# Kernel tuning notes

Measured on AMD Instinct MI355X. Metric: run time of the kernel, lower is better.

The kernel has to match this reference:

```python
import jax, jax.numpy as jnp
import numpy as np

NUM_BRANCHES = 4
REP_DIM = 1024
FEAT_DIM = 128
N_DATA = 100000
NCE_K = 4096
NCE_T = 0.07
BATCH = 128
EPS = 1e-07


def setup_inputs() -> dict:
    key = jax.random.key(0)
    ks = jax.random.split(key, 8)
    d = {}
    for i in range(NUM_BRANCHES):
        d[f"emb{i}"] = jax.random.normal(ks[i], (BATCH, REP_DIM), dtype=jnp.float32)
    d["W"] = jax.random.normal(ks[4], (NUM_BRANCHES, FEAT_DIM, REP_DIM), dtype=jnp.float32) * 0.03
    d["b"] = jnp.zeros((NUM_BRANCHES, FEAT_DIM), dtype=jnp.float32)
    stdv = 1.0 / np.sqrt(FEAT_DIM / 3.0)
    d["memory"] = jax.random.uniform(ks[5], (NUM_BRANCHES, N_DATA, FEAT_DIM), dtype=jnp.float32, minval=-stdv, maxval=stdv)
    idx = jax.random.randint(ks[6], (BATCH,), 0, N_DATA)
    neg = jax.random.randint(ks[7], (BATCH, NCE_K), 0, N_DATA)
    d["idx"] = idx
    d["contrast_idx"] = jnp.concatenate([idx[:, None], neg], axis=1)  # col 0 = positive
    return d


def reference(emb0, emb1, emb2, emb3, W, b, memory, idx, contrast_idx):
    # per-branch Embed: flatten -> Linear -> L2 normalize
    embs = jnp.stack([emb0, emb1, emb2, emb3], axis=0)            # [R,B,rep]
    h = jnp.einsum('rbi,rdi->rbd', embs, W) + b[:, None, :]        # [R,B,D]
    e = h / jnp.sqrt(jnp.sum(h * h, axis=-1, keepdims=True))       # Normalize(power=2)

    # ContrastMemory: gather K+1 bank rows per sample per branch (detached)
    w = jax.lax.stop_gradient(memory[:, contrast_idx, :])          # [R,B,K+1,D]
    # scores[i,j,b,k] = <bank_j row, emb_i>  for every ordered pair
    scores = jnp.einsum('jbkd,ibd->ijbk', w, e)                    # [R,R,B,K+1]
    out = jnp.exp(scores / NCE_T)
    Z = jax.lax.stop_gradient(jnp.mean(out, axis=(2, 3)) * N_DATA)  # per-pair Z estimate
    out = out / Z[:, :, None, None]

    # ContrastLoss (Eq 11)
    m = float(NCE_K)
    Pn = 1.0 / float(N_DATA)
    pos = out[:, :, :, 0]                                          # [R,R,B]
    neg = out[:, :, :, 1:]                                         # [R,R,B,K]
    log_D1 = jnp.log(pos / (pos + m * Pn + EPS))
    log_D0 = jnp.log((m * Pn) / (neg + m * Pn + EPS))
    per_pair = -(jnp.sum(log_D1, axis=2) + jnp.sum(log_D0, axis=(2, 3))) / BATCH
    mask = 1.0 - jnp.eye(NUM_BRANCHES, dtype=per_pair.dtype)       # only i != j pairs
    return jnp.sum(per_pair * mask)
```

## Files before the change

### kernel.cpp

```cpp
#include <hip/hip_runtime.h>
#include <math.h>

#define NBR    4
#define REP    1024
#define FD     128
#define NDATA  100000
#define KP1    4097
#define BN     128
#define MPN    0.04096f
#define EPS_C  1e-7f
#define TINV   (1.0f / 0.07f)
#define NSLOT  64

typedef unsigned int   uint4e   __attribute__((ext_vector_type(4)));
typedef unsigned short ushort4e __attribute__((ext_vector_type(4)));

static __device__ __forceinline__ unsigned short bfbits(unsigned int u) {
    u += 0x7fffu + ((u >> 16) & 1u);
    return (unsigned short)(u >> 16);
}
static __device__ __forceinline__ unsigned short f2bf(float f) {
    union { float f; unsigned int u; } c; c.f = f;
    return bfbits(c.u);
}
static __device__ __forceinline__ float bf2f(unsigned short h) {
    union { unsigned int u; float f; } c; c.u = ((unsigned int)h) << 16;
    return c.f;
}
static __device__ __forceinline__ float lo_of(unsigned int u) {
    union { unsigned int u; float f; } c; c.u = u << 16; return c.f;
}
static __device__ __forceinline__ float hi_of(unsigned int u) {
    union { unsigned int u; float f; } c; c.u = u & 0xffff0000u; return c.f;
}

__global__ void k_convert_t(const float* __restrict__ src, ushort* __restrict__ dst) {
    const size_t t = (size_t)blockIdx.x * 256 + threadIdx.x;
    const size_t total = (size_t)NBR * NDATA * 32;
    if (t >= total) return;
    unsigned int jn = (unsigned int)(t >> 5);
    unsigned int q  = (unsigned int)(t & 31);
    unsigned int j  = jn / (unsigned int)NDATA;
    unsigned int n  = jn - j * (unsigned int)NDATA;
    uint4e v = __builtin_nontemporal_load((const uint4e*)src + t);
    ushort4e o;
    o.x = bfbits(v.x); o.y = bfbits(v.y); o.z = bfbits(v.z); o.w = bfbits(v.w);
    ((ushort4e*)dst)[((size_t)n * NBR + j) * 32 + q] = o;
}

__global__ void k_feat(const float* __restrict__ e0, const float* __restrict__ e1,
                       const float* __restrict__ e2, const float* __restrict__ e3,
                       const float* __restrict__ W, const float* __restrict__ bias,
                       float* __restrict__ e_out) {
    const int r = blockIdx.x;
    const int b = blockIdx.y;
    const float* emb = (r == 0 ? e0 : r == 1 ? e1 : r == 2 ? e2 : e3) + (size_t)b * REP;

    __shared__ float s_emb[REP];
    for (int i = threadIdx.x; i < REP; i += blockDim.x) s_emb[i] = emb[i];
    __syncthreads();

    const int d = threadIdx.x;
    const float4* wrow = (const float4*)(W + ((size_t)r * FD + d) * REP);
    float acc = 0.f;
#pragma unroll 8
    for (int c = 0; c < REP / 4; ++c) {
        float4 v = wrow[c];
        acc += v.x * s_emb[4*c+0] + v.y * s_emb[4*c+1]
             + v.z * s_emb[4*c+2] + v.w * s_emb[4*c+3];
    }
    float h = acc + bias[r * FD + d];

    __shared__ float red[FD];
    red[d] = h * h;
    __syncthreads();
    for (int off = FD / 2; off > 0; off >>= 1) {
        if (d < off) red[d] += red[d + off];
        __syncthreads();
    }
    float nrm = sqrtf(red[0]);
    e_out[((size_t)r * BN + b) * FD + d] = h / nrm;
}

__global__ __launch_bounds__(256)
void k_pass1w(const float* __restrict__ e, const ushort* __restrict__ memT,
              const int* __restrict__ cidx, float* __restrict__ Zsl,
              ushort* __restrict__ expS) {
    const int b    = blockIdx.y;
    const int lane = threadIdx.x & 63;
    const int w    = threadIdx.x >> 6;
    const int wid  = w + (blockIdx.x << 2);
    const int nw   = gridDim.x << 2;
    const int j    = lane >> 4;
    const int d0   = (lane & 15) * 8;

    float er[4][8];
#pragma unroll
    for (int i = 0; i < 4; ++i) {
        const float4* ep = (const float4*)(e + ((size_t)i * BN + b) * FD + d0);
        float4 v0 = ep[0], v1 = ep[1];
        er[i][0] = v0.x; er[i][1] = v0.y; er[i][2] = v0.z; er[i][3] = v0.w;
        er[i][4] = v1.x; er[i][5] = v1.y; er[i][6] = v1.z; er[i][7] = v1.w;
    }

    const int*   ci  = cidx + (size_t)b * KP1;
    const uint4* mt  = (const uint4*)memT;
    ushort*      esb = expS + (size_t)b * (KP1 * 16);

    float z0 = 0.f, z1 = 0.f, z2 = 0.f, z3 = 0.f;

    int k = wid;
    uint4 buf;
    if (k < KP1) {
        int n = ci[k];
        buf = mt[(size_t)n * 64 + lane];
    }
    while (k < KP1) {
        const int k2 = k + nw;
        uint4 cur = buf;
        if (k2 < KP1) {
            int n2 = ci[k2];
            buf = mt[(size_t)n2 * 64 + lane];
        }

        float a0 = 0.f, a1 = 0.f, a2 = 0.f, a3 = 0.f;
#pragma unroll
        for (int q = 0; q < 4; ++q) {
            unsigned int u = (&cur.x)[q];
            float wl = lo_of(u), wh = hi_of(u);
            a0 += wl * er[0][q*2] + wh * er[0][q*2+1];
            a1 += wl * er[1][q*2] + wh * er[1][q*2+1];
            a2 += wl * er[2][q*2] + wh * er[2][q*2+1];
            a3 += wl * er[3][q*2] + wh * er[3][q*2+1];
        }
#pragma unroll
        for (int off = 1; off < 16; off <<= 1) {
            a0 += __shfl_xor(a0, off, 64);
            a1 += __shfl_xor(a1, off, 64);
            a2 += __shfl_xor(a2, off, 64);
            a3 += __shfl_xor(a3, off, 64);
        }
        float x0 = __expf(a0 * TINV), x1 = __expf(a1 * TINV);
        float x2 = __expf(a2 * TINV), x3 = __expf(a3 * TINV);
        z0 += x0; z1 += x1; z2 += x2; z3 += x3;

        if ((lane & 15) == 0) {
            ushort4e st;
            st.x = f2bf(x0); st.y = f2bf(x1); st.z = f2bf(x2); st.w = f2bf(x3);
            *(ushort4e*)(esb + (size_t)k * 16 + j * 4) = st;
        }
        k = k2;
    }

    __shared__ float s_z[4][16];
    if ((lane & 15) == 0) {
        s_z[w][0*4 + j] = z0;
        s_z[w][1*4 + j] = z1;
        s_z[w][2*4 + j] = z2;
        s_z[w][3*4 + j] = z3;
    }
    __syncthreads();
    if (threadIdx.x < 16) {
        float v = s_z[0][threadIdx.x] + s_z[1][threadIdx.x]
                + s_z[2][threadIdx.x] + s_z[3][threadIdx.x];
        const int slot = (blockIdx.y * gridDim.x + blockIdx.x) & (NSLOT - 1);
        atomicAdd(&Zsl[slot * 16 + threadIdx.x], v);
    }
}

__global__ void k_zred(const float* __restrict__ Zsl, float* __restrict__ Zsum) {
    if (threadIdx.x < 16) {
        float s = 0.f;
        for (int sl = 0; sl < NSLOT; ++sl) s += Zsl[sl * 16 + threadIdx.x];
        Zsum[threadIdx.x] = s;
    }
}

static __device__ __forceinline__ void acc_words(unsigned int w0, unsigned int w1,
                                                 unsigned int w2, unsigned int w3,
                                                 unsigned int w4, unsigned int w5,
                                                 unsigned int w6, unsigned int w7,
                                                 const float* __restrict__ s_zinv,
                                                 float* __restrict__ acc, bool pos) {
    unsigned int wds[8] = {w0, w1, w2, w3, w4, w5, w6, w7};
#pragma unroll
    for (int w = 0; w < 8; ++w) {
        float v0 = lo_of(wds[w]) * s_zinv[2*w];
        float v1 = hi_of(wds[w]) * s_zinv[2*w+1];
        if (pos) {
            acc[2*w]   += -__logf(1.f + (MPN + EPS_C) / v0);
            acc[2*w+1] += -__logf(1.f + (MPN + EPS_C) / v1);
        } else {
            acc[2*w]   += -__logf(1.f + (v0 + EPS_C) * (1.f / MPN));
            acc[2*w+1] += -__logf(1.f + (v1 + EPS_C) * (1.f / MPN));
        }
    }
}

__global__ __launch_bounds__(256)
void k_pass2f(const uint4* __restrict__ expS, const float* __restrict__ Zsum,
              float* __restrict__ Asl) {
    const int b = blockIdx.y;

    __shared__ float s_zinv[16];
    if (threadIdx.x < 16) {
        int jj = threadIdx.x >> 2, ii = threadIdx.x & 3;
        float Z = Zsum[ii * 4 + jj] *
                  (float)((double)NDATA / ((double)BN * (double)KP1));
        s_zinv[threadIdx.x] = 1.0f / Z;
    }
    __syncthreads();

    const uint4* es = expS + (size_t)b * (KP1 * 2);
    const int base = threadIdx.x + blockIdx.x * 256;

    float acc[16];
#pragma unroll
    for (int t = 0; t < 16; ++t) acc[t] = 0.f;

#pragma unroll
    for (int it = 0; it < 2; ++it) {
        const int k = base + it * 2048;
        uint4 p0 = es[(size_t)k * 2];
        uint4 p1 = es[(size_t)k * 2 + 1];
        acc_words(p0.x, p0.y, p0.z, p0.w, p1.x, p1.y, p1.z, p1.w,
                  s_zinv, acc, k == 0);
    }
    if (base == 0) {
        uint4 p0 = es[(size_t)4096 * 2];
        uint4 p1 = es[(size_t)4096 * 2 + 1];
        acc_words(p0.x, p0.y, p0.z, p0.w, p1.x, p1.y, p1.z, p1.w,
                  s_zinv, acc, false);
    }

#pragma unroll
    for (int t = 0; t < 16; ++t) {
#pragma unroll
        for (int off = 32; off > 0; off >>= 1)
            acc[t] += __shfl_down(acc[t], off, 64);
    }
    __shared__ float s_a[4][16];
    const int w = threadIdx.x >> 6;
    if ((threadIdx.x & 63) == 0) {
#pragma unroll
        for (int t = 0; t < 16; ++t) s_a[w][t] = acc[t];
    }
    __syncthreads();
    if (threadIdx.x < 16) {
        float v = s_a[0][threadIdx.x] + s_a[1][threadIdx.x]
                + s_a[2][threadIdx.x] + s_a[3][threadIdx.x];
        const int slot = (blockIdx.y * gridDim.x + blockIdx.x) & (NSLOT - 1);
        atomicAdd(&Asl[slot * 16 + threadIdx.x], v);
    }
}

__global__ void k_final_slots(const float* __restrict__ Asl, float* __restrict__ out) {
    const int tid = threadIdx.x;
    const int comp = tid & 15;
    const int grp  = tid >> 4;
    float a = 0.f;
    for (int sl = grp; sl < NSLOT; sl += 16) a += Asl[sl * 16 + comp];
    const float m = ((comp >> 2) != (comp & 3)) ? 1.f : 0.f;
    __shared__ float s[256];
    s[tid] = a * m;
    __syncthreads();
    for (int off = 128; off > 0; off >>= 1) {
        if (tid < off) s[tid] += s[tid + off];
        __syncthreads();
    }
    if (tid == 0) out[0] = -s[0] / (float)BN;
}

static __device__ __forceinline__ void dot4(const float4* __restrict__ row,
                                            const float* __restrict__ se,
                                            float& a0, float& a1, float& a2, float& a3) {
    a0 = a1 = a2 = a3 = 0.f;
#pragma unroll 8
    for (int c = 0; c < FD / 4; ++c) {
        float4 v = row[c];
        const int o = 4 * c;
        a0 += v.x * se[0*FD+o+0] + v.y * se[0*FD+o+1] + v.z * se[0*FD+o+2] + v.w * se[0*FD+o+3];
        a1 += v.x * se[1*FD+o+0] + v.y * se[1*FD+o+1] + v.z * se[1*FD+o+2] + v.w * se[1*FD+o+3];
        a2 += v.x * se[2*FD+o+0] + v.y * se[2*FD+o+1] + v.z * se[2*FD+o+2] + v.w * se[2*FD+o+3];
        a3 += v.x * se[3*FD+o+0] + v.y * se[3*FD+o+1] + v.z * se[3*FD+o+2] + v.w * se[3*FD+o+3];
    }
}

static __device__ __forceinline__ void block_reduce4(float z0, float z1, float z2,
                                                     float z3, float* dst, int j) {
    __shared__ float sred[256];
    float zs[NBR] = {z0, z1, z2, z3};
    for (int i = 0; i < NBR; ++i) {
        sred[threadIdx.x] = zs[i];
        __syncthreads();
        for (int off = 128; off > 0; off >>= 1) {
            if ((int)threadIdx.x < off) sred[threadIdx.x] += sred[threadIdx.x + off];
            __syncthreads();
        }
        if (threadIdx.x == 0) atomicAdd(&dst[i * NBR + j], sred[0]);
        __syncthreads();
    }
}

static __device__ __forceinline__ float term_of(float ex, float zinv, int k) {
    const float c = MPN + EPS_C;
    float v = ex * zinv;
    if (k == 0) return -__logf(1.0f + c / v);
    return -__logf(1.0f + (v + EPS_C) * (1.0f / MPN));
}

template <bool STORE>
__global__ void k_pass1_f32(const float* __restrict__ e, const float* __restrict__ memory,
                            const int* __restrict__ cidx,
                            float* __restrict__ Zsum, ushort4* __restrict__ expS) {
    const int j = blockIdx.z;
    const int b = blockIdx.y;

    __shared__ float s_e[NBR * FD];
    for (int t = threadIdx.x; t < NBR * FD; t += blockDim.x) {
        int i = t >> 7, d = t & (FD - 1);
        s_e[t] = e[((size_t)i * BN + b) * FD + d];
    }
    __syncthreads();

    const int* ci = cidx + (size_t)b * KP1;
    const float4* mem4 = (const float4*)(memory + (size_t)j * NDATA * FD);
    float z0 = 0.f, z1 = 0.f, z2 = 0.f, z3 = 0.f;

    for (int k = threadIdx.x + blockIdx.x * blockDim.x; k < KP1;
         k += blockDim.x * gridDim.x) {
        const int n = ci[k];
        const float4* row = mem4 + (size_t)n * (FD / 4);
        float a0, a1, a2, a3;
        dot4(row, s_e, a0, a1, a2, a3);
        float x0 = __expf(a0 * TINV);
        float x1 = __expf(a1 * TINV);
        float x2 = __expf(a2 * TINV);
        float x3 = __expf(a3 * TINV);
        z0 += x0; z1 += x1; z2 += x2; z3 += x3;
        if (STORE) {
            ushort4 st;
            st.x = f2bf(x0); st.y = f2bf(x1); st.z = f2bf(x2); st.w = f2bf(x3);
            expS[((size_t)j * BN + b) * KP1 + k] = st;
        }
    }
    block_reduce4(z0, z1, z2, z3, Zsum, j);
}

__global__ void k_pass2_stored(const ushort4* __restrict__ expS,
                               const float* __restrict__ Zsum,
                               float* __restrict__ accum) {
    const int j = blockIdx.z;
    const int b = blockIdx.y;

    __shared__ float s_zinv[NBR];
    if (threadIdx.x < NBR) {
        float Z = Zsum[threadIdx.x * NBR + j] *
                  (float)((double)NDATA / ((double)BN * (double)KP1));
        s_zinv[threadIdx.x] = 1.0f / Z;
    }
    __syncthreads();

    const ushort4* es = expS + ((size_t)j * BN + b) * KP1;
    float a0 = 0.f, a1 = 0.f, a2 = 0.f, a3 = 0.f;

    for (int k = threadIdx.x + blockIdx.x * blockDim.x; k < KP1;
         k += blockDim.x * gridDim.x) {
        ushort4 v = es[k];
        a0 += term_of(bf2f(v.x), s_zinv[0], k);
        a1 += term_of(bf2f(v.y), s_zinv[1], k);
        a2 += term_of(bf2f(v.z), s_zinv[2], k);
        a3 += term_of(bf2f(v.w), s_zinv[3], k);
    }
    block_reduce4(a0, a1, a2, a3, accum, j);
}

__global__ void k_pass2_regather(const float* __restrict__ e, const float* __restrict__ memory,
                                 const int* __restrict__ cidx,
                                 const float* __restrict__ Zsum, float* __restrict__ accum) {
    const int j = blockIdx.z;
    const int b = blockIdx.y;

    __shared__ float s_e[NBR * FD];
    __shared__ float s_zinv[NBR];
    for (int t = threadIdx.x; t < NBR * FD; t += blockDim.x) {
        int i = t >> 7, d = t & (FD - 1);
        s_e[t] = e[((size_t)i * BN + b) * FD + d];
    }
    if (threadIdx.x < NBR) {
        float Z = Zsum[threadIdx.x * NBR + j] *
                  (float)((double)NDATA / ((double)BN * (double)KP1));
        s_zinv[threadIdx.x] = 1.0f / Z;
    }
    __syncthreads();

    const int* ci = cidx + (size_t)b * KP1;
    const float4* mem4 = (const float4*)(memory + (size_t)j * NDATA * FD);
    float a0s = 0.f, a1s = 0.f, a2s = 0.f, a3s = 0.f;

    for (int k = threadIdx.x + blockIdx.x * blockDim.x; k < KP1;
         k += blockDim.x * gridDim.x) {
        const int n = ci[k];
        const float4* row = mem4 + (size_t)n * (FD / 4);
        float a0, a1, a2, a3;
        dot4(row, s_e, a0, a1, a2, a3);
        a0s += term_of(__expf(a0 * TINV), s_zinv[0], k);
        a1s += term_of(__expf(a1 * TINV), s_zinv[1], k);
        a2s += term_of(__expf(a2 * TINV), s_zinv[2], k);
        a3s += term_of(__expf(a3 * TINV), s_zinv[3], k);
    }
    block_reduce4(a0s, a1s, a2s, a3s, accum, j);
}

__global__ void k_init(float* __restrict__ p, int n) {
    int i = blockIdx.x * blockDim.x + threadIdx.x;
    if (i < n) p[i] = 0.f;
}

__global__ void k_final_legacy(const float* __restrict__ accum, float* __restrict__ out) {
    if (threadIdx.x == 0) {
        float s = 0.f;
        for (int i = 0; i < NBR; ++i)
            for (int j = 0; j < NBR; ++j)
                if (i != j) s += -accum[i * NBR + j] / (float)BN;
        out[0] = s;
    }
}

extern "C" void kernel_launch(void* const* d_in, const int* in_sizes, int n_in,
                              void* d_out, int out_size, void* d_ws, size_t ws_size,
                              hipStream_t stream) {
    const float* e0   = (const float*)d_in[0];
    const float* e1   = (const float*)d_in[1];
    const float* e2   = (const float*)d_in[2];
    const float* e3   = (const float*)d_in[3];
    const float* W    = (const float*)d_in[4];
    const float* bias = (const float*)d_in[5];
    const float* mem  = (const float*)d_in[6];
    const int*   cidx = (const int*)d_in[8];
    float* out = (float*)d_out;

    float* ws    = (float*)d_ws;
    float* e     = ws;
    float* Zsum  = ws + 65536;
    float* accum = ws + 65552;
    float* Zsl   = ws + 65568;
    float* Asl   = ws + 66592;
    const size_t base_b = (size_t)67616 * 4;
    const size_t memT_b = (size_t)NDATA * NBR * FD * 2;
    const size_t expS_b = (size_t)BN * KP1 * 16 * 2;

    const size_t need_full = base_b + memT_b + expS_b;
    const size_t need_mid  = base_b + expS_b;

    k_init<<<9, 256, 0, stream>>>(Zsum, 2080);
    k_feat<<<dim3(NBR, BN), 128, 0, stream>>>(e0, e1, e2, e3, W, bias, e);

    if (ws_size >= need_full) {
        ushort* memT = (ushort*)((char*)d_ws + base_b);
        ushort* expS = (ushort*)((char*)d_ws + base_b + memT_b);
        k_convert_t<<<50000, 256, 0, stream>>>(mem, memT);
        k_pass1w<<<dim3(16, BN), 256, 0, stream>>>(e, memT, cidx, Zsl, expS);
        k_zred<<<1, 64, 0, stream>>>(Zsl, Zsum);
        k_pass2f<<<dim3(8, BN), 256, 0, stream>>>((const uint4*)expS, Zsum, Asl);
        k_final_slots<<<1, 256, 0, stream>>>(Asl, out);
    } else if (ws_size >= need_mid) {
        ushort4* expS = (ushort4*)((char*)d_ws + base_b);
        k_pass1_f32<true><<<dim3(4, BN, NBR), 256, 0, stream>>>(e, mem, cidx, Zsum, expS);
        k_pass2_stored<<<dim3(4, BN, NBR), 256, 0, stream>>>(expS, Zsum, accum);
        k_final_legacy<<<1, 64, 0, stream>>>(accum, out);
    } else {
        k_pass1_f32<false><<<dim3(4, BN, NBR), 256, 0, stream>>>(e, mem, cidx, Zsum, nullptr);
        k_pass2_regather<<<dim3(4, BN, NBR), 256, 0, stream>>>(e, mem, cidx, Zsum, accum);
        k_final_legacy<<<1, 64, 0, stream>>>(accum, out);
    }
}
```

Baseline: 473.0 us.

## Use fp16 bank with packed fdot2, transpose-reduce shuffles and deeper prefetch

The transposed memory bank and the stored exp scores switch from bf16 to fp16. The pass-1 gather kernel now computes its dot products with packed fp16 fdot2 instructions against fp16 copies of the embeddings. A transpose-style butterfly replaces the four independent 16-lane shuffle reductions, so each lane ends up owning one (i,j) score, which cuts shuffle and exp work. Gather prefetch now runs two iterations ahead instead of one. The cost is fp16 range: exp(score/T) overflows once a score exceeds about 0.77, and the embeddings lose some precision.

```diff
diff --git a/kernel.cpp b/kernel.cpp
--- a/kernel.cpp
+++ b/kernel.cpp
@@ -14,24 +14,29 @@
 
 typedef unsigned int   uint4e   __attribute__((ext_vector_type(4)));
 typedef unsigned short ushort4e __attribute__((ext_vector_type(4)));
-
-static __device__ __forceinline__ unsigned short bfbits(unsigned int u) {
+typedef _Float16       half2e   __attribute__((ext_vector_type(2)));
+
+static __device__ __forceinline__ unsigned short f2h(float f) {
+    union { _Float16 h; unsigned short u; } c; c.h = (_Float16)f; return c.u;
+}
+static __device__ __forceinline__ float h_lo(unsigned int u) {
+    union { unsigned int u; _Float16 h[2]; } c; c.u = u; return (float)c.h[0];
+}
+static __device__ __forceinline__ float h_hi(unsigned int u) {
+    union { unsigned int u; _Float16 h[2]; } c; c.u = u; return (float)c.h[1];
+}
+static __device__ __forceinline__ half2e u2h2(unsigned int u) {
+    union { unsigned int u; half2e h; } c; c.u = u; return c.h;
+}
+static __device__ __forceinline__ unsigned short f2bf(float f) {
+    union { float f; unsigned int u; } c; c.f = f;
+    unsigned int u = c.u;
     u += 0x7fffu + ((u >> 16) & 1u);
     return (unsigned short)(u >> 16);
-}
-static __device__ __forceinline__ unsigned short f2bf(float f) {
-    union { float f; unsigned int u; } c; c.f = f;
-    return bfbits(c.u);
 }
 static __device__ __forceinline__ float bf2f(unsigned short h) {
     union { unsigned int u; float f; } c; c.u = ((unsigned int)h) << 16;
     return c.f;
-}
-static __device__ __forceinline__ float lo_of(unsigned int u) {
-    union { unsigned int u; float f; } c; c.u = u << 16; return c.f;
-}
-static __device__ __forceinline__ float hi_of(unsigned int u) {
-    union { unsigned int u; float f; } c; c.u = u & 0xffff0000u; return c.f;
 }
 
 __global__ void k_convert_t(const float* __restrict__ src, ushort* __restrict__ dst) {
@@ -43,8 +48,10 @@
     unsigned int j  = jn / (unsigned int)NDATA;
     unsigned int n  = jn - j * (unsigned int)NDATA;
     uint4e v = __builtin_nontemporal_load((const uint4e*)src + t);
+    union { unsigned int u; float f; } c0, c1, c2, c3;
+    c0.u = v.x; c1.u = v.y; c2.u = v.z; c3.u = v.w;
     ushort4e o;
-    o.x = bfbits(v.x); o.y = bfbits(v.y); o.z = bfbits(v.z); o.w = bfbits(v.w);
+    o.x = f2h(c0.f); o.y = f2h(c1.f); o.z = f2h(c2.f); o.w = f2h(c3.f);
     ((ushort4e*)dst)[((size_t)n * NBR + j) * 32 + q] = o;
 }
 
@@ -91,74 +98,66 @@
     const int w    = threadIdx.x >> 6;
     const int wid  = w + (blockIdx.x << 2);
     const int nw   = gridDim.x << 2;
-    const int j    = lane >> 4;
-    const int d0   = (lane & 15) * 8;
-
-    float er[4][8];
+    const int l4   = lane & 15;
+    const int d0   = l4 * 8;
+    const bool b3  = (l4 & 8) != 0;
+    const bool b2  = (l4 & 4) != 0;
+
+    half2e eh[4][4];
 #pragma unroll
     for (int i = 0; i < 4; ++i) {
         const float4* ep = (const float4*)(e + ((size_t)i * BN + b) * FD + d0);
         float4 v0 = ep[0], v1 = ep[1];
-        er[i][0] = v0.x; er[i][1] = v0.y; er[i][2] = v0.z; er[i][3] = v0.w;
-        er[i][4] = v1.x; er[i][5] = v1.y; er[i][6] = v1.z; er[i][7] = v1.w;
+        eh[i][0] = half2e{(_Float16)v0.x, (_Float16)v0.y};
+        eh[i][1] = half2e{(_Float16)v0.z, (_Float16)v0.w};
+        eh[i][2] = half2e{(_Float16)v1.x, (_Float16)v1.y};
+        eh[i][3] = half2e{(_Float16)v1.z, (_Float16)v1.w};
     }
 
     const int*   ci  = cidx + (size_t)b * KP1;
     const uint4* mt  = (const uint4*)memT;
     ushort*      esb = expS + (size_t)b * (KP1 * 16);
 
-    float z0 = 0.f, z1 = 0.f, z2 = 0.f, z3 = 0.f;
+    float z = 0.f;
 
     int k = wid;
-    uint4 buf;
-    if (k < KP1) {
-        int n = ci[k];
-        buf = mt[(size_t)n * 64 + lane];
-    }
-    while (k < KP1) {
-        const int k2 = k + nw;
-        uint4 cur = buf;
-        if (k2 < KP1) {
-            int n2 = ci[k2];
-            buf = mt[(size_t)n2 * 64 + lane];
+    uint4 A, B;
+    if (k < KP1)      A = mt[(size_t)ci[k] * 64 + lane];
+    if (k + nw < KP1) B = mt[(size_t)ci[k + nw] * 64 + lane];
+
+    for (; k < KP1; k += nw) {
+        uint4 cur = A;
+        A = B;
+        const int kpf = k + 2 * nw;
+        if (kpf < KP1) B = mt[(size_t)ci[kpf] * 64 + lane];
+
+        float a0 = 0.f, a1 = 0.f, a2 = 0.f, a3 = 0.f;
+#pragma unroll
+        for (int q = 0; q < 4; ++q) {
+            half2e hw = u2h2((&cur.x)[q]);
+            a0 = __builtin_amdgcn_fdot2(hw, eh[0][q], a0, false);
+            a1 = __builtin_amdgcn_fdot2(hw, eh[1][q], a1, false);
+            a2 = __builtin_amdgcn_fdot2(hw, eh[2][q], a2, false);
+            a3 = __builtin_amdgcn_fdot2(hw, eh[3][q], a3, false);
         }
-
-        float a0 = 0.f, a1 = 0.f, a2 = 0.f, a3 = 0.f;
-#pragma unroll
-        for (int q = 0; q < 4; ++q) {
-            unsigned int u = (&cur.x)[q];
-            float wl = lo_of(u), wh = hi_of(u);
-            a0 += wl * er[0][q*2] + wh * er[0][q*2+1];
-            a1 += wl * er[1][q*2] + wh * er[1][q*2+1];
-            a2 += wl * er[2][q*2] + wh * er[2][q*2+1];
-            a3 += wl * er[3][q*2] + wh * er[3][q*2+1];
-        }
-#pragma unroll
-        for (int off = 1; off < 16; off <<= 1) {
-            a0 += __shfl_xor(a0, off, 64);
-            a1 += __shfl_xor(a1, off, 64);
-            a2 += __shfl_xor(a2, off, 64);
-            a3 += __shfl_xor(a3, off, 64);
-        }
-        float x0 = __expf(a0 * TINV), x1 = __expf(a1 * TINV);
-        float x2 = __expf(a2 * TINV), x3 = __expf(a3 * TINV);
-        z0 += x0; z1 += x1; z2 += x2; z3 += x3;
-
-        if ((lane & 15) == 0) {
-            ushort4e st;
-            st.x = f2bf(x0); st.y = f2bf(x1); st.z = f2bf(x2); st.w = f2bf(x3);
-            *(ushort4e*)(esb + (size_t)k * 16 + j * 4) = st;
-        }
-        k = k2;
+        float t0 = __shfl_xor(b3 ? a0 : a2, 8, 64);
+        float t1 = __shfl_xor(b3 ? a1 : a3, 8, 64);
+        float c0 = (b3 ? a2 : a0) + t0;
+        float c1 = (b3 ? a3 : a1) + t1;
+        float t2 = __shfl_xor(b2 ? c0 : c1, 4, 64);
+        float d  = (b2 ? c1 : c0) + t2;
+        d += __shfl_xor(d, 2, 64);
+        d += __shfl_xor(d, 1, 64);
+        float x = __expf(d * TINV);
+        z += x;
+        if ((lane & 3) == 0)
+            esb[(size_t)k * 16 + (lane >> 2)] = f2h(x);
     }
 
     __shared__ float s_z[4][16];
-    if ((lane & 15) == 0) {
-        s_z[w][0*4 + j] = z0;
-        s_z[w][1*4 + j] = z1;
-        s_z[w][2*4 + j] = z2;
-        s_z[w][3*4 + j] = z3;
-    }
+    const int j = lane >> 4;
+    const int i = ((l4 >> 3) << 1) | ((l4 >> 2) & 1);
+    if ((lane & 3) == 0) s_z[w][i * 4 + j] = z;
     __syncthreads();
     if (threadIdx.x < 16) {
         float v = s_z[0][threadIdx.x] + s_z[1][threadIdx.x]
@@ -176,17 +175,14 @@
     }
 }
 
-static __device__ __forceinline__ void acc_words(unsigned int w0, unsigned int w1,
-                                                 unsigned int w2, unsigned int w3,
-                                                 unsigned int w4, unsigned int w5,
-                                                 unsigned int w6, unsigned int w7,
+static __device__ __forceinline__ void acc_words(const uint4& p0, const uint4& p1,
                                                  const float* __restrict__ s_zinv,
                                                  float* __restrict__ acc, bool pos) {
-    unsigned int wds[8] = {w0, w1, w2, w3, w4, w5, w6, w7};
+    unsigned int wds[8] = {p0.x, p0.y, p0.z, p0.w, p1.x, p1.y, p1.z, p1.w};
 #pragma unroll
     for (int w = 0; w < 8; ++w) {
-        float v0 = lo_of(wds[w]) * s_zinv[2*w];
-        float v1 = hi_of(wds[w]) * s_zinv[2*w+1];
+        float v0 = h_lo(wds[w]) * s_zinv[2*w];
+        float v1 = h_hi(wds[w]) * s_zinv[2*w+1];
         if (pos) {
             acc[2*w]   += -__logf(1.f + (MPN + EPS_C) / v0);
             acc[2*w+1] += -__logf(1.f + (MPN + EPS_C) / v1);
@@ -223,14 +219,12 @@
         const int k = base + it * 2048;
         uint4 p0 = es[(size_t)k * 2];
         uint4 p1 = es[(size_t)k * 2 + 1];
-        acc_words(p0.x, p0.y, p0.z, p0.w, p1.x, p1.y, p1.z, p1.w,
-                  s_zinv, acc, k == 0);
+        acc_words(p0, p1, s_zinv, acc, k == 0);
     }
     if (base == 0) {
         uint4 p0 = es[(size_t)4096 * 2];
         uint4 p1 = es[(size_t)4096 * 2 + 1];
-        acc_words(p0.x, p0.y, p0.z, p0.w, p1.x, p1.y, p1.z, p1.w,
-                  s_zinv, acc, false);
+        acc_words(p0, p1, s_zinv, acc, false);
     }
 
 #pragma unroll
```

After: 426.6 us. -9.8%, faster.
